# Optimization experiments

Measured on AMD Instinct MI355X. Metric: run time of the kernel, lower is better.

## Reference

```python
import jax, jax.numpy as jnp
import numpy as np

B, D3, L, H, O, E, GH = 4096, 288, 32, 512, 96, 8, 128


def _init_linear(key, out_dim, in_dim):
    kw, kb = jax.random.split(key)
    bound = 1.0 / np.sqrt(in_dim)
    W = jax.random.uniform(kw, (out_dim, in_dim), jnp.float32, -bound, bound)
    b = jax.random.uniform(kb, (out_dim,), jnp.float32, -bound, bound)
    return W, b


def setup_inputs() -> dict:
    key = jax.random.key(0)
    ks = jax.random.split(key, 12)
    x = jax.random.normal(ks[0], (B, D3), jnp.float32)
    z = jax.random.normal(ks[1], (B, L), jnp.float32)
    # per-expert weights, stacked on leading expert axis [E, out, in]
    def expert_stack(k, out_dim, in_dim):
        Ws, bs = [], []
        for i in range(E):
            Wi, bi = _init_linear(jax.random.fold_in(k, i), out_dim, in_dim)
            Ws.append(Wi); bs.append(bi)
        return jnp.stack(Ws), jnp.stack(bs)
    W0, b0 = expert_stack(ks[2], H, D3 + L)
    W1, b1 = expert_stack(ks[3], H, H + L)
    W2, b2 = expert_stack(ks[4], H, H + L)
    W3, b3 = expert_stack(ks[5], O, H)
    gW1, gb1 = _init_linear(ks[6], GH, D3 + L)
    gW2, gb2 = _init_linear(ks[7], GH, GH)
    gW3, gb3 = _init_linear(ks[8], E, GH)
    return {"x": x, "z": z, "W0": W0, "b0": b0, "W1": W1, "b1": b1,
            "W2": W2, "b2": b2, "W3": W3, "b3": b3,
            "gW1": gW1, "gb1": gb1, "gW2": gW2, "gb2": gb2,
            "gW3": gW3, "gb3": gb3}


def _gating(x, z, gW1, gb1, gW2, gb2, gW3, gb3):
    h = jnp.concatenate([x, z], axis=1)
    h = jax.nn.elu(h @ gW1.T + gb1)
    h = jax.nn.elu(h @ gW2.T + gb2)
    return jax.nn.softmax(h @ gW3.T + gb3, axis=-1)  # [B, E]


def _blended_linear(g, W, b, h):
    # Original: materializes sum_e g[b,e] * W_e -> [B,out,in], then bmm.
    # Mathematically identical linear form: sum_e g[b,e] * (W_e h_b + b_e).
    return jnp.einsum('be,eoi,bi->bo', g, W, h) + g @ b


def reference(x, z, W0, b0, W1, b1, W2, b2, W3, b3,
              gW1, gb1, gW2, gb2, gW3, gb3):
    g = _gating(x, z, gW1, gb1, gW2, gb2, gW3, gb3)  # [B, E]
    # dropout p=0.0 (eval) -> identity
    h = jax.nn.elu(_blended_linear(g, W0, b0, jnp.concatenate([x, z], axis=1)))
    h = jax.nn.elu(_blended_linear(g, W1, b1, jnp.concatenate([h, z], axis=1)))
    h = jax.nn.elu(_blended_linear(g, W2, b2, jnp.concatenate([h, z], axis=1)))
    out = _blended_linear(g, W3, b3, h)
    return out  # [B, O]
```

## Files before the change

### kernel.cpp

```cpp
#include <hip/hip_runtime.h>
#include <hip/hip_fp16.h>

typedef _Float16 half8 __attribute__((ext_vector_type(8)));
typedef _Float16 half4 __attribute__((ext_vector_type(4)));
typedef float floatx4 __attribute__((ext_vector_type(4)));

__device__ __forceinline__ void async_ld16(const void* g, void* l) {
    __builtin_amdgcn_global_load_lds(
        (const __attribute__((address_space(1))) char*)g,
        (__attribute__((address_space(3))) char*)l, 16, 0, 0);
}

__device__ __forceinline__ float elu_f(float v) {
    return v > 0.f ? v : expm1f(v);
}

__device__ __forceinline__ half4 cvt4(const float* src, int j4) {
    float4 f = ((const float4*)src)[j4];
    half4 h; h.x = (_Float16)f.x; h.y = (_Float16)f.y;
    h.z = (_Float16)f.z; h.w = (_Float16)f.w; return h;
}

__device__ __forceinline__ half8 cvt8(const float* src) {
    float4 f0 = ((const float4*)src)[0];
    float4 f1 = ((const float4*)src)[1];
    half8 h;
    h[0] = (_Float16)f0.x; h[1] = (_Float16)f0.y; h[2] = (_Float16)f0.z; h[3] = (_Float16)f0.w;
    h[4] = (_Float16)f1.x; h[5] = (_Float16)f1.y; h[6] = (_Float16)f1.z; h[7] = (_Float16)f1.w;
    return h;
}

__launch_bounds__(256)
__global__ void gating_and_wconv(const float* __restrict__ x, const float* __restrict__ z,
                                 const float* __restrict__ gW1, const float* __restrict__ gW2,
                                 const float* __restrict__ gW3,
                                 const float* __restrict__ gb1, const float* __restrict__ gb2,
                                 const float* __restrict__ gb3,
                                 float* __restrict__ g,
                                 const float* __restrict__ W0, const float* __restrict__ W1,
                                 const float* __restrict__ W2, const float* __restrict__ W3,
                                 _Float16* __restrict__ X0,
                                 _Float16* __restrict__ h0, _Float16* __restrict__ h1,
                                 _Float16* __restrict__ h2,
                                 _Float16* __restrict__ Wc0, _Float16* __restrict__ Wc1,
                                 _Float16* __restrict__ Wc2, _Float16* __restrict__ Wc3)
{
    const int tid = threadIdx.x;

    if (blockIdx.x >= 32) {
        const int S0 = 294912;
        const int S1 = 32768;
        const int S2 = 327680;
        const int S3 = 589824;
        const int S4 = 589824;
        const int S5 = 98304;
        const int S6 = 196608;
        const int TOTAL = S0 + S1 + S2 + S3 + S4 + S5 + S6;
        const int nb = gridDim.x - 32;
        const half4 hz = {};
        for (int i = (blockIdx.x - 32) * blockDim.x + tid; i < TOTAL;
             i += nb * blockDim.x) {
            int j = i;
            if (j < S0) {
                int r = j / 72, c = j - r * 72;
                *(half4*)(X0 + r * 320 + c * 4) = cvt4(x, j);
                continue;
            }
            j -= S0;
            if (j < S1) {
                int r = j / 8, c = j - r * 8;
                *(half4*)(X0 + r * 320 + 288 + c * 4) = cvt4(z, j);
                continue;
            }
            j -= S1;
            if (j < S2) { *(half4*)(Wc0 + j * 4) = cvt4(W0, j); continue; }
            j -= S2;
            if (j < S3) {
                int r = j / 144, c = j - r * 144;
                *(half4*)(Wc1 + r * 576 + c * 4) = (c < 136) ? cvt4(W1, r * 136 + c) : hz;
                continue;
            }
            j -= S3;
            if (j < S4) {
                int r = j / 144, c = j - r * 144;
                *(half4*)(Wc2 + r * 576 + c * 4) = (c < 136) ? cvt4(W2, r * 136 + c) : hz;
                continue;
            }
            j -= S4;
            if (j < S5) { *(half4*)(Wc3 + j * 4) = cvt4(W3, j); continue; }
            j -= S5;
            int buf = j >> 16;
            int r2 = j & 65535;
            int row = r2 >> 4, c = r2 & 15;
            _Float16* h = (buf == 0) ? h0 : ((buf == 1) ? h1 : h2);
            *(half4*)(h + row * 576 + 512 + c * 4) = (c < 8) ? cvt4(z, row * 8 + c) : hz;
        }
        return;
    }

    __shared__ _Float16 sA[128 * 32];
    __shared__ _Float16 sB[128 * 32];
    __shared__ _Float16 h1t[128 * 136];
    __shared__ _Float16 sW3[8 * 128];

    const int l = tid & 63;
    const int w = tid >> 6;
    const int wm = w >> 1, wn = w & 1;
    const int m0 = blockIdx.x * 128;

    for (int t = tid; t < 8 * 128; t += 256) sW3[t] = (_Float16)gW3[t];

    const int sub = l >> 2;
    const int kc  = (l & 3) * 8;
    const int row0 = w * 16 + sub;

    const int mi = l & 15, quad = l >> 4;
    const _Float16* rA = sA + (wm * 64 + mi) * 32 + quad * 8;
    const _Float16* rB = sB + (wn * 64 + mi) * 32 + quad * 8;

    floatx4 acc[4][4] = {};

    for (int k0 = 0; k0 < 320; k0 += 32) {
        half8 a0, a1, b0, b1;
        if (k0 < 288) {
            a0 = cvt8(x + (size_t)(m0 + row0) * 288 + k0 + kc);
            a1 = cvt8(x + (size_t)(m0 + row0 + 64) * 288 + k0 + kc);
        } else {
            a0 = cvt8(z + (size_t)(m0 + row0) * 32 + kc);
            a1 = cvt8(z + (size_t)(m0 + row0 + 64) * 32 + kc);
        }
        b0 = cvt8(gW1 + (size_t)row0 * 320 + k0 + kc);
        b1 = cvt8(gW1 + (size_t)(row0 + 64) * 320 + k0 + kc);
        __syncthreads();
        *(half8*)(sA + row0 * 32 + kc) = a0;
        *(half8*)(sA + (row0 + 64) * 32 + kc) = a1;
        *(half8*)(sB + row0 * 32 + kc) = b0;
        *(half8*)(sB + (row0 + 64) * 32 + kc) = b1;
        __syncthreads();
        half8 af[4], bf[4];
#pragma unroll
        for (int i = 0; i < 4; i++) af[i] = *(const half8*)(rA + i * 16 * 32);
#pragma unroll
        for (int j = 0; j < 4; j++) bf[j] = *(const half8*)(rB + j * 16 * 32);
#pragma unroll
        for (int i = 0; i < 4; i++)
#pragma unroll
            for (int j = 0; j < 4; j++)
                acc[i][j] = __builtin_amdgcn_mfma_f32_16x16x32_f16(af[i], bf[j], acc[i][j], 0, 0, 0);
    }
    __syncthreads();
#pragma unroll
    for (int i = 0; i < 4; i++)
#pragma unroll
        for (int j = 0; j < 4; j++) {
            int n = wn * 64 + j * 16 + mi;
            float bn = gb1[n];
#pragma unroll
            for (int r = 0; r < 4; r++) {
                int mrel = wm * 64 + i * 16 + quad * 4 + r;
                h1t[mrel * 136 + n] = (_Float16)elu_f(acc[i][j][r] + bn);
            }
        }

    floatx4 acc2[4][4] = {};
    const _Float16* rA2b = h1t + (wm * 64 + mi) * 136 + quad * 8;
    for (int ks = 0; ks < 4; ks++) {
        half8 b0 = cvt8(gW2 + (size_t)row0 * 128 + ks * 32 + kc);
        half8 b1 = cvt8(gW2 + (size_t)(row0 + 64) * 128 + ks * 32 + kc);
        __syncthreads();
        *(half8*)(sB + row0 * 32 + kc) = b0;
        *(half8*)(sB + (row0 + 64) * 32 + kc) = b1;
        __syncthreads();
        half8 af[4], bf[4];
#pragma unroll
        for (int i = 0; i < 4; i++) af[i] = *(const half8*)(rA2b + i * 16 * 136 + ks * 32);
#pragma unroll
        for (int j = 0; j < 4; j++) bf[j] = *(const half8*)(rB + j * 16 * 32);
#pragma unroll
        for (int i = 0; i < 4; i++)
#pragma unroll
            for (int j = 0; j < 4; j++)
                acc2[i][j] = __builtin_amdgcn_mfma_f32_16x16x32_f16(af[i], bf[j], acc2[i][j], 0, 0, 0);
    }
    __syncthreads();
#pragma unroll
    for (int i = 0; i < 4; i++)
#pragma unroll
        for (int j = 0; j < 4; j++) {
            int n = wn * 64 + j * 16 + mi;
            float bn = gb2[n];
#pragma unroll
            for (int r = 0; r < 4; r++) {
                int mrel = wm * 64 + i * 16 + quad * 4 + r;
                h1t[mrel * 136 + n] = (_Float16)elu_f(acc2[i][j][r] + bn);
            }
        }
    __syncthreads();

    const int e = l >> 3, kk = l & 7;
    for (int rr = 0; rr < 32; rr++) {
        int row = w * 32 + rr;
        const _Float16* hr = h1t + row * 136 + kk * 16;
        const _Float16* wr = sW3 + e * 128 + kk * 16;
        half8 hv0 = *(const half8*)hr;
        half8 hv1 = *(const half8*)(hr + 8);
        half8 wv0 = *(const half8*)wr;
        half8 wv1 = *(const half8*)(wr + 8);
        float s = 0.f;
#pragma unroll
        for (int t = 0; t < 8; t++)
            s += (float)hv0[t] * (float)wv0[t] + (float)hv1[t] * (float)wv1[t];
        s += __shfl_xor(s, 1);
        s += __shfl_xor(s, 2);
        s += __shfl_xor(s, 4);
        float logit = s + gb3[e];
        float mx = logit;
        mx = fmaxf(mx, __shfl_xor(mx, 8));
        mx = fmaxf(mx, __shfl_xor(mx, 16));
        mx = fmaxf(mx, __shfl_xor(mx, 32));
        float ve = __expf(logit - mx);
        float ssum = ve;
        ssum += __shfl_xor(ssum, 1);
        ssum += __shfl_xor(ssum, 2);
        ssum += __shfl_xor(ssum, 4);
        ssum += __shfl_xor(ssum, 8);
        ssum += __shfl_xor(ssum, 16);
        ssum += __shfl_xor(ssum, 32);
        float gv = ve / (ssum * 0.125f);
        if (kk == 0) g[(size_t)(m0 + row) * 8 + e] = gv;
    }
}

template <bool ELU_ACT, typename OUT_T>
__launch_bounds__(256, 4)
__global__ void blend64(const _Float16* __restrict__ A, int lda,
                        const _Float16* __restrict__ W, int ldw,
                        int Hdim, int K,
                        const float* __restrict__ g,
                        const float* __restrict__ bias,
                        OUT_T* __restrict__ out, int ldo)
{
    __shared__ __align__(16) char smem_raw[32768];
    _Float16* sA = (_Float16*)smem_raw;
    _Float16* sB = (_Float16*)(smem_raw + 16384);
    float* sredf = (float*)smem_raw;
    __shared__ float sg[128][9];
    __shared__ float sbias[8][16];

    const int tid = threadIdx.x;
    const int l = tid & 63;
    const int w = tid >> 6;
    const int wm = w >> 1, wn = w & 1;
    const int o0 = blockIdx.x * 16;
    const int m0 = blockIdx.y * 128;

    for (int t = tid; t < 128 * 8; t += 256)
        sg[t >> 3][t & 7] = g[(size_t)(m0 + (t >> 3)) * 8 + (t & 7)];
    for (int t = tid; t < 128; t += 256)
        sbias[t >> 4][t & 15] = bias[(t >> 4) * Hdim + o0 + (t & 15)];

    const int lr = l >> 3;
    const int lc = l & 7;
    const int swz = lc ^ lr;

    const _Float16* gAp = A + (size_t)(m0 + w * 64 + lr) * lda + swz * 8;
    _Float16* lAp = sA + w * 4096;
    const int wb = w - 2;
    const int eb = wb * 4;
    const _Float16* gBe = W + ((size_t)eb * Hdim + o0 + lr) * ldw + swz * 8;
    const _Float16* gBo = gBe + (size_t)8 * ldw;
    _Float16* lBp = sB + wb * 4096;

    const int mi = l & 15, quad = l >> 4;
    const int cswz = mi & 7;
    const int offh0 = ((quad ^ cswz) * 8);
    const int offh1 = (((quad + 4) ^ cswz) * 8);
    const _Float16* rAb = sA + (wm * 64 + mi) * 64;
    const _Float16* rBb = sB + (wn * 64 + mi) * 64;

    floatx4 acc[4][4] = {};

    for (int k0 = 0; k0 < K; k0 += 64) {
        __syncthreads();
        if (w < 2) {
            const _Float16* gp = gAp + k0;
            _Float16* lp = lAp;
#pragma unroll
            for (int c = 0; c < 8; c++) {
                async_ld16(gp, lp);
                gp += (size_t)8 * lda;
                lp += 512;
            }
        } else {
            const _Float16* ge = gBe + k0;
            const _Float16* go = gBo + k0;
            _Float16* lp = lBp;
#pragma unroll
            for (int c2 = 0; c2 < 4; c2++) {
                async_ld16(ge, lp); lp += 512;
                async_ld16(go, lp); lp += 512;
                ge += (size_t)Hdim * ldw;
                go += (size_t)Hdim * ldw;
            }
        }
        __syncthreads();
#pragma unroll
        for (int h = 0; h < 2; h++) {
            const int off = h ? offh1 : offh0;
            half8 af[4], bf[4];
#pragma unroll
            for (int i = 0; i < 4; i++) af[i] = *(const half8*)(rAb + i * 1024 + off);
#pragma unroll
            for (int j = 0; j < 4; j++) bf[j] = *(const half8*)(rBb + j * 1024 + off);
#pragma unroll
            for (int i = 0; i < 4; i++)
#pragma unroll
                for (int j = 0; j < 4; j++)
                    acc[i][j] = __builtin_amdgcn_mfma_f32_16x16x32_f16(af[i], bf[j], acc[i][j], 0, 0, 0);
        }
    }

    float p[4][4];
#pragma unroll
    for (int i = 0; i < 4; i++)
#pragma unroll
        for (int r = 0; r < 4; r++) {
            int mloc = wm * 64 + i * 16 + quad * 4 + r;
            float s = 0.f;
#pragma unroll
            for (int j = 0; j < 4; j++) {
                int e = wn * 4 + j;
                s += sg[mloc][e] * (acc[i][j][r] + sbias[e][mi]);
            }
            p[i][r] = s;
        }

    __syncthreads();
    if (wn == 0) {
#pragma unroll
        for (int i = 0; i < 4; i++)
#pragma unroll
            for (int r = 0; r < 4; r++)
                sredf[(wm * 64 + i * 16 + quad * 4 + r) * 17 + mi] = p[i][r];
    }
    __syncthreads();
    if (wn == 1) {
#pragma unroll
        for (int i = 0; i < 4; i++)
#pragma unroll
            for (int r = 0; r < 4; r++) {
                int mrel = i * 16 + quad * 4 + r;
                float v = p[i][r] + sredf[(wm * 64 + mrel) * 17 + mi];
                if (ELU_ACT) v = elu_f(v);
                out[(size_t)(m0 + wm * 64 + mrel) * ldo + o0 + mi] = (OUT_T)v;
            }
    }
}

extern "C" void kernel_launch(void* const* d_in, const int* in_sizes, int n_in,
                              void* d_out, int out_size, void* d_ws, size_t ws_size,
                              hipStream_t stream)
{
    (void)in_sizes; (void)n_in; (void)out_size; (void)ws_size;
    const float* x   = (const float*)d_in[0];
    const float* z   = (const float*)d_in[1];
    const float* W0  = (const float*)d_in[2];
    const float* b0  = (const float*)d_in[3];
    const float* W1  = (const float*)d_in[4];
    const float* b1  = (const float*)d_in[5];
    const float* W2  = (const float*)d_in[6];
    const float* b2  = (const float*)d_in[7];
    const float* W3  = (const float*)d_in[8];
    const float* b3  = (const float*)d_in[9];
    const float* gW1 = (const float*)d_in[10];
    const float* gb1 = (const float*)d_in[11];
    const float* gW2 = (const float*)d_in[12];
    const float* gb2 = (const float*)d_in[13];
    const float* gW3 = (const float*)d_in[14];
    const float* gb3 = (const float*)d_in[15];

    char* p = (char*)d_ws;
    auto alloc = [&](size_t n) { char* r = p; p += (n + 255) & ~(size_t)255; return r; };
    _Float16* X0   = (_Float16*)alloc((size_t)4096 * 320 * 2);
    _Float16* h0   = (_Float16*)alloc((size_t)4096 * 576 * 2);
    _Float16* h1   = (_Float16*)alloc((size_t)4096 * 576 * 2);
    _Float16* h2   = (_Float16*)alloc((size_t)4096 * 576 * 2);
    _Float16* Wc0  = (_Float16*)alloc((size_t)8 * 512 * 320 * 2);
    _Float16* Wc1  = (_Float16*)alloc((size_t)8 * 512 * 576 * 2);
    _Float16* Wc2  = (_Float16*)alloc((size_t)8 * 512 * 576 * 2);
    _Float16* Wc3  = (_Float16*)alloc((size_t)8 * 96 * 512 * 2);
    float*    g    = (float*)alloc((size_t)4096 * 8 * 4);

    gating_and_wconv<<<1024, 256, 0, stream>>>(x, z, gW1, gW2, gW3, gb1, gb2, gb3, g,
                                               W0, W1, W2, W3, X0, h0, h1, h2,
                                               Wc0, Wc1, Wc2, Wc3);

    blend64<true, _Float16><<<dim3(32, 32), 256, 0, stream>>>(X0, 320, Wc0, 320, 512, 320, g, b0, h0, 576);
    blend64<true, _Float16><<<dim3(32, 32), 256, 0, stream>>>(h0, 576, Wc1, 576, 512, 576, g, b1, h1, 576);
    blend64<true, _Float16><<<dim3(32, 32), 256, 0, stream>>>(h1, 576, Wc2, 576, 512, 576, g, b2, h2, 576);
    blend64<false, float><<<dim3(6, 32), 256, 0, stream>>>(h2, 576, Wc3, 512, 96, 512, g, b3, (float*)d_out, 96);
}
```

Measured before the change: 224.3 us.

## Restructure gating MLP into per-wave 16-row MFMA tiles across more blocks

The gating MLP now runs on 64 blocks instead of 32. Each wave owns 16 rows and runs all three layers with MFMA, keeping intermediates in a private LDS tile, so no block-wide barriers are needed. The old scalar dot-product path for the final gate layer is replaced by an MFMA whose B operand is half zero-padded. ELU switches from expm1f to __expf(v)-1, which is cheaper but less accurate near zero. In exchange, weight fragments are re-read from global memory per wave rather than shared through LDS, and fewer blocks remain for the weight-conversion work.

```diff
diff --git a/kernel.cpp b/kernel.cpp
--- a/kernel.cpp
+++ b/kernel.cpp
@@ -12,7 +12,7 @@
 }
 
 __device__ __forceinline__ float elu_f(float v) {
-    return v > 0.f ? v : expm1f(v);
+    return v > 0.f ? v : (__expf(v) - 1.f);
 }
 
 __device__ __forceinline__ half4 cvt4(const float* src, int j4) {
@@ -31,23 +31,25 @@
 }
 
 __launch_bounds__(256)
-__global__ void gating_and_wconv(const float* __restrict__ x, const float* __restrict__ z,
-                                 const float* __restrict__ gW1, const float* __restrict__ gW2,
-                                 const float* __restrict__ gW3,
-                                 const float* __restrict__ gb1, const float* __restrict__ gb2,
-                                 const float* __restrict__ gb3,
-                                 float* __restrict__ g,
-                                 const float* __restrict__ W0, const float* __restrict__ W1,
-                                 const float* __restrict__ W2, const float* __restrict__ W3,
-                                 _Float16* __restrict__ X0,
-                                 _Float16* __restrict__ h0, _Float16* __restrict__ h1,
-                                 _Float16* __restrict__ h2,
-                                 _Float16* __restrict__ Wc0, _Float16* __restrict__ Wc1,
-                                 _Float16* __restrict__ Wc2, _Float16* __restrict__ Wc3)
+__global__ void gating_conv(const float* __restrict__ x, const float* __restrict__ z,
+                            const float* __restrict__ gW1, const float* __restrict__ gW2,
+                            const float* __restrict__ gW3,
+                            const float* __restrict__ gb1, const float* __restrict__ gb2,
+                            const float* __restrict__ gb3,
+                            float* __restrict__ g,
+                            const float* __restrict__ W0, const float* __restrict__ W1,
+                            const float* __restrict__ W2, const float* __restrict__ W3,
+                            _Float16* __restrict__ X0,
+                            _Float16* __restrict__ h0, _Float16* __restrict__ h1,
+                            _Float16* __restrict__ h2,
+                            _Float16* __restrict__ Wc0, _Float16* __restrict__ Wc1,
+                            _Float16* __restrict__ Wc2, _Float16* __restrict__ Wc3)
 {
+    __shared__ _Float16 Tbuf[4 * 2 * 16 * 136];
+
     const int tid = threadIdx.x;
 
-    if (blockIdx.x >= 32) {
+    if (blockIdx.x >= 64) {
         const int S0 = 294912;
         const int S1 = 32768;
         const int S2 = 327680;
@@ -56,9 +58,9 @@
         const int S5 = 98304;
         const int S6 = 196608;
         const int TOTAL = S0 + S1 + S2 + S3 + S4 + S5 + S6;
-        const int nb = gridDim.x - 32;
+        const int nb = gridDim.x - 64;
         const half4 hz = {};
-        for (int i = (blockIdx.x - 32) * blockDim.x + tid; i < TOTAL;
+        for (int i = (blockIdx.x - 64) * blockDim.x + tid; i < TOTAL;
              i += nb * blockDim.x) {
             int j = i;
             if (j < S0) {
@@ -98,136 +100,79 @@
         return;
     }
 
-    __shared__ _Float16 sA[128 * 32];
-    __shared__ _Float16 sB[128 * 32];
-    __shared__ _Float16 h1t[128 * 136];
-    __shared__ _Float16 sW3[8 * 128];
-
     const int l = tid & 63;
     const int w = tid >> 6;
-    const int wm = w >> 1, wn = w & 1;
-    const int m0 = blockIdx.x * 128;
-
-    for (int t = tid; t < 8 * 128; t += 256) sW3[t] = (_Float16)gW3[t];
-
-    const int sub = l >> 2;
-    const int kc  = (l & 3) * 8;
-    const int row0 = w * 16 + sub;
-
-    const int mi = l & 15, quad = l >> 4;
-    const _Float16* rA = sA + (wm * 64 + mi) * 32 + quad * 8;
-    const _Float16* rB = sB + (wn * 64 + mi) * 32 + quad * 8;
-
-    floatx4 acc[4][4] = {};
-
-    for (int k0 = 0; k0 < 320; k0 += 32) {
-        half8 a0, a1, b0, b1;
-        if (k0 < 288) {
-            a0 = cvt8(x + (size_t)(m0 + row0) * 288 + k0 + kc);
-            a1 = cvt8(x + (size_t)(m0 + row0 + 64) * 288 + k0 + kc);
-        } else {
-            a0 = cvt8(z + (size_t)(m0 + row0) * 32 + kc);
-            a1 = cvt8(z + (size_t)(m0 + row0 + 64) * 32 + kc);
-        }
-        b0 = cvt8(gW1 + (size_t)row0 * 320 + k0 + kc);
-        b1 = cvt8(gW1 + (size_t)(row0 + 64) * 320 + k0 + kc);
-        __syncthreads();
-        *(half8*)(sA + row0 * 32 + kc) = a0;
-        *(half8*)(sA + (row0 + 64) * 32 + kc) = a1;
-        *(half8*)(sB + row0 * 32 + kc) = b0;
-        *(half8*)(sB + (row0 + 64) * 32 + kc) = b1;
-        __syncthreads();
-        half8 af[4], bf[4];
-#pragma unroll
-        for (int i = 0; i < 4; i++) af[i] = *(const half8*)(rA + i * 16 * 32);
-#pragma unroll
-        for (int j = 0; j < 4; j++) bf[j] = *(const half8*)(rB + j * 16 * 32);
-#pragma unroll
-        for (int i = 0; i < 4; i++)
-#pragma unroll
-            for (int j = 0; j < 4; j++)
-                acc[i][j] = __builtin_amdgcn_mfma_f32_16x16x32_f16(af[i], bf[j], acc[i][j], 0, 0, 0);
-    }
-    __syncthreads();
-#pragma unroll
-    for (int i = 0; i < 4; i++)
-#pragma unroll
-        for (int j = 0; j < 4; j++) {
-            int n = wn * 64 + j * 16 + mi;
-            float bn = gb1[n];
-#pragma unroll
-            for (int r = 0; r < 4; r++) {
-                int mrel = wm * 64 + i * 16 + quad * 4 + r;
-                h1t[mrel * 136 + n] = (_Float16)elu_f(acc[i][j][r] + bn);
-            }
-        }
-
-    floatx4 acc2[4][4] = {};
-    const _Float16* rA2b = h1t + (wm * 64 + mi) * 136 + quad * 8;
-    for (int ks = 0; ks < 4; ks++) {
-        half8 b0 = cvt8(gW2 + (size_t)row0 * 128 + ks * 32 + kc);
-        half8 b1 = cvt8(gW2 + (size_t)(row0 + 64) * 128 + ks * 32 + kc);
-        __syncthreads();
-        *(half8*)(sB + row0 * 32 + kc) = b0;
-        *(half8*)(sB + (row0 + 64) * 32 + kc) = b1;
-        __syncthreads();
-        half8 af[4], bf[4];
-#pragma unroll
-        for (int i = 0; i < 4; i++) af[i] = *(const half8*)(rA2b + i * 16 * 136 + ks * 32);
-#pragma unroll
-        for (int j = 0; j < 4; j++) bf[j] = *(const half8*)(rB + j * 16 * 32);
-#pragma unroll
-        for (int i = 0; i < 4; i++)
-#pragma unroll
-            for (int j = 0; j < 4; j++)
-                acc2[i][j] = __builtin_amdgcn_mfma_f32_16x16x32_f16(af[i], bf[j], acc2[i][j], 0, 0, 0);
-    }
-    __syncthreads();
-#pragma unroll
-    for (int i = 0; i < 4; i++)
-#pragma unroll
-        for (int j = 0; j < 4; j++) {
-            int n = wn * 64 + j * 16 + mi;
-            float bn = gb2[n];
-#pragma unroll
-            for (int r = 0; r < 4; r++) {
-                int mrel = wm * 64 + i * 16 + quad * 4 + r;
-                h1t[mrel * 136 + n] = (_Float16)elu_f(acc2[i][j][r] + bn);
-            }
-        }
-    __syncthreads();
-
-    const int e = l >> 3, kk = l & 7;
-    for (int rr = 0; rr < 32; rr++) {
-        int row = w * 32 + rr;
-        const _Float16* hr = h1t + row * 136 + kk * 16;
-        const _Float16* wr = sW3 + e * 128 + kk * 16;
-        half8 hv0 = *(const half8*)hr;
-        half8 hv1 = *(const half8*)(hr + 8);
-        half8 wv0 = *(const half8*)wr;
-        half8 wv1 = *(const half8*)(wr + 8);
-        float s = 0.f;
-#pragma unroll
-        for (int t = 0; t < 8; t++)
-            s += (float)hv0[t] * (float)wv0[t] + (float)hv1[t] * (float)wv1[t];
+    const int quad = l >> 4;
+    const int mi = l & 15;
+    const int kq = quad * 8;
+    const int mrow = (blockIdx.x * 4 + w) * 16;
+
+    _Float16* T1 = Tbuf + w * (2 * 16 * 136);
+    _Float16* T2 = T1 + 16 * 136;
+
+    floatx4 acc1[8] = {};
+    for (int kc = 0; kc < 10; kc++) {
+        const int k0 = kc * 32;
+        half8 a = (k0 < 288) ? cvt8(x + (size_t)(mrow + mi) * 288 + k0 + kq)
+                             : cvt8(z + (size_t)(mrow + mi) * 32 + kq);
+#pragma unroll
+        for (int t = 0; t < 8; t++) {
+            half8 b = cvt8(gW1 + (size_t)(t * 16 + mi) * 320 + k0 + kq);
+            acc1[t] = __builtin_amdgcn_mfma_f32_16x16x32_f16(a, b, acc1[t], 0, 0, 0);
+        }
+    }
+#pragma unroll
+    for (int t = 0; t < 8; t++) {
+        const int n = t * 16 + mi;
+        const float bn = gb1[n];
+#pragma unroll
+        for (int r = 0; r < 4; r++)
+            T1[(quad * 4 + r) * 136 + n] = (_Float16)elu_f(acc1[t][r] + bn);
+    }
+
+    floatx4 acc2[8] = {};
+#pragma unroll
+    for (int kc = 0; kc < 4; kc++) {
+        const int k0 = kc * 32;
+        half8 a = *(const half8*)(T1 + mi * 136 + k0 + kq);
+#pragma unroll
+        for (int t = 0; t < 8; t++) {
+            half8 b = cvt8(gW2 + (size_t)(t * 16 + mi) * 128 + k0 + kq);
+            acc2[t] = __builtin_amdgcn_mfma_f32_16x16x32_f16(a, b, acc2[t], 0, 0, 0);
+        }
+    }
+#pragma unroll
+    for (int t = 0; t < 8; t++) {
+        const int n = t * 16 + mi;
+        const float bn = gb2[n];
+#pragma unroll
+        for (int r = 0; r < 4; r++)
+            T2[(quad * 4 + r) * 136 + n] = (_Float16)elu_f(acc2[t][r] + bn);
+    }
+
+    floatx4 acc3 = {};
+#pragma unroll
+    for (int kc = 0; kc < 4; kc++) {
+        const int k0 = kc * 32;
+        half8 a = *(const half8*)(T2 + mi * 136 + k0 + kq);
+        half8 b = (mi < 8) ? cvt8(gW3 + (size_t)mi * 128 + k0 + kq) : half8{};
+        acc3 = __builtin_amdgcn_mfma_f32_16x16x32_f16(a, b, acc3, 0, 0, 0);
+    }
+    const float gb = gb3[mi & 7];
+#pragma unroll
+    for (int r = 0; r < 4; r++) {
+        float logit = acc3[r] + gb;
+        float mx = logit;
+        mx = fmaxf(mx, __shfl_xor(mx, 1));
+        mx = fmaxf(mx, __shfl_xor(mx, 2));
+        mx = fmaxf(mx, __shfl_xor(mx, 4));
+        float e = __expf(logit - mx);
+        float s = e;
         s += __shfl_xor(s, 1);
         s += __shfl_xor(s, 2);
         s += __shfl_xor(s, 4);
-        float logit = s + gb3[e];
-        float mx = logit;
-        mx = fmaxf(mx, __shfl_xor(mx, 8));
-        mx = fmaxf(mx, __shfl_xor(mx, 16));
-        mx = fmaxf(mx, __shfl_xor(mx, 32));
-        float ve = __expf(logit - mx);
-        float ssum = ve;
-        ssum += __shfl_xor(ssum, 1);
-        ssum += __shfl_xor(ssum, 2);
-        ssum += __shfl_xor(ssum, 4);
-        ssum += __shfl_xor(ssum, 8);
-        ssum += __shfl_xor(ssum, 16);
-        ssum += __shfl_xor(ssum, 32);
-        float gv = ve / (ssum * 0.125f);
-        if (kk == 0) g[(size_t)(m0 + row) * 8 + e] = gv;
+        if (mi < 8)
+            g[(size_t)(mrow + quad * 4 + r) * 8 + mi] = e / s;
     }
 }
 
@@ -391,9 +336,9 @@
     _Float16* Wc3  = (_Float16*)alloc((size_t)8 * 96 * 512 * 2);
     float*    g    = (float*)alloc((size_t)4096 * 8 * 4);
 
-    gating_and_wconv<<<1024, 256, 0, stream>>>(x, z, gW1, gW2, gW3, gb1, gb2, gb3, g,
-                                               W0, W1, W2, W3, X0, h0, h1, h2,
-                                               Wc0, Wc1, Wc2, Wc3);
+    gating_conv<<<1024, 256, 0, stream>>>(x, z, gW1, gW2, gW3, gb1, gb2, gb3, g,
+                                          W0, W1, W2, W3, X0, h0, h1, h2,
+                                          Wc0, Wc1, Wc2, Wc3);
 
     blend64<true, _Float16><<<dim3(32, 32), 256, 0, stream>>>(X0, 320, Wc0, 320, 512, 320, g, b0, h0, 576);
     blend64<true, _Float16><<<dim3(32, 32), 256, 0, stream>>>(h0, 576, Wc1, 576, 512, 576, g, b1, h1, 576);
```

Measured after the change: 223.7 us. No clear change (-0.3%).
